# Optimization experiments

Hardware: AMD Instinct MI355X
Metric: run time of the kernel (lower is better)

The kernel has to match this reference:

```python
import jax, jax.numpy as jnp
import numpy as np

# --- config (matches init_kwargs) ---
NUM_EXPERTS = 8
TOP_K = 2
GROUP_DET = 1024
GROUP_CLS = 512
D_MODEL = 768
MLP_DIM = 3072


def setup_inputs() -> dict:
    key = jax.random.key(0)
    ks = jax.random.split(key, 8)
    scale = 0.02
    return {
        "x_det": jax.random.normal(ks[0], (16, 1024, D_MODEL), dtype=jnp.float32),
        "x_cls": jax.random.normal(ks[1], (16, 256, D_MODEL), dtype=jnp.float32),
        "w_router_det": jax.random.normal(ks[2], (D_MODEL, NUM_EXPERTS), dtype=jnp.float32) * scale,
        "w_router_cls": jax.random.normal(ks[3], (D_MODEL, NUM_EXPERTS), dtype=jnp.float32) * scale,
        "w1": jax.random.normal(ks[4], (NUM_EXPERTS, D_MODEL, MLP_DIM), dtype=jnp.float32) * scale,
        "b1": jnp.zeros((NUM_EXPERTS, MLP_DIM), dtype=jnp.float32),
        "w2": jax.random.normal(ks[5], (NUM_EXPERTS, MLP_DIM, D_MODEL), dtype=jnp.float32) * scale,
        "b2": jnp.zeros((NUM_EXPERTS, D_MODEL), dtype=jnp.float32),
    }


def _route(xg, w_router, top_k, num_experts, capacity):
    """Top-k per-item routing with expert capacity (vmoe-style einsum dispatcher).

    xg: [G, S, D] grouped tokens. Returns dispatch [G,S,E,C], combine [G,S,E,C].
    """
    G, S, _ = xg.shape
    gates = jax.nn.softmax(jnp.einsum("gsd,de->gse", xg, w_router))  # [G,S,E]
    gval, gidx = jax.lax.top_k(gates, top_k)  # [G,S,k]
    # k-major ordering: slot-0 choices of all tokens get capacity priority.
    mask = jax.nn.one_hot(gidx, num_experts, dtype=xg.dtype)  # [G,S,k,E]
    mask = mask.transpose(0, 2, 1, 3).reshape(G, top_k * S, num_experts)
    pos = jnp.cumsum(mask, axis=1) - 1.0  # position within expert buffer
    keep = mask * (pos < capacity)
    disp = keep[..., None] * jax.nn.one_hot(pos, capacity, dtype=xg.dtype)  # [G,kS,E,C]
    disp = disp.reshape(G, top_k, S, num_experts, capacity)
    combine = jnp.einsum("gksec,gks->gsec", disp, gval.transpose(0, 2, 1))
    dispatch = disp.sum(axis=1)  # [G,S,E,C] (one-hot: a token goes to each expert <=1 time)
    return dispatch, combine


def _expert_mlp(expert_in, w1, b1, w2, b2):
    # expert_in: [E, N, D] -> vmapped-expert MLP (grouped GEMM)
    h = jax.nn.gelu(jnp.einsum("end,edh->enh", expert_in, w1) + b1[:, None, :])
    return jnp.einsum("enh,ehd->end", h, w2) + b2[:, None, :]


def _moe(x, w_router, w1, b1, w2, b2, group_size):
    B, S, D = x.shape
    G = (B * S) // group_size
    capacity = (TOP_K * group_size) // NUM_EXPERTS
    xg = x.reshape(G, group_size, D)
    dispatch, combine = _route(xg, w_router, TOP_K, NUM_EXPERTS, capacity)
    expert_in = jnp.einsum("gsec,gsd->egcd", dispatch, xg)  # [E,G,C,D]
    E, _, C, _ = expert_in.shape
    y = _expert_mlp(expert_in.reshape(E, G * C, D), w1, b1, w2, b2).reshape(E, G, C, D)
    out = jnp.einsum("gsec,egcd->gsd", combine, y)
    return out.reshape(B, S, D)


def reference(x_det, x_cls, w_router_det, w_router_cls, w1, b1, w2, b2):
    out_det = _moe(x_det, w_router_det, w1, b1, w2, b2, GROUP_DET)
    out_cls = _moe(x_cls, w_router_cls, w1, b1, w2, b2, GROUP_CLS)
    # concatenate the two streams along the sequence axis for a single output
    return jnp.concatenate([out_det, out_cls], axis=1)
```

## Files before the change

### kernel.cpp

```cpp
#include <hip/hip_runtime.h>
#include <cstdint>
#include <cstddef>

#define NE 8
#define DMODEL 768
#define MLPDIM 3072
#define NDET 16384
#define NCLS 4096
#define NTOK 20480
#define ROWS_PER_E 5120
#define TOT_ROWS 40960

typedef float f32x4 __attribute__((ext_vector_type(4)));
typedef __bf16 bf16x8 __attribute__((ext_vector_type(8)));

__device__ __forceinline__ unsigned short f2bf(float f) {
    unsigned u = __float_as_uint(f);
    u += 0x7FFFu + ((u >> 16) & 1u);
    return (unsigned short)(u >> 16);
}
__device__ __forceinline__ float bf2f(unsigned v) {
    return __uint_as_float(v << 16);
}
__device__ __forceinline__ float gelu_f(float x) {
    float u = x * (0.7978845608028654f + 0.0356774081099f * x * x);
    return x * __frcp_rn(1.0f + __expf(-2.0f * u));
}

__device__ __forceinline__ void gload16(const void* g, void* l) {
    __builtin_amdgcn_global_load_lds(
        (const __attribute__((address_space(1))) unsigned int*)g,
        (__attribute__((address_space(3))) unsigned int*)l, 16, 0, 0);
}

__global__ void k_router(const float* __restrict__ xd, const float* __restrict__ xc,
                         const float* __restrict__ wrd, const float* __restrict__ wrc,
                         ushort* __restrict__ xbf,
                         int* __restrict__ e1, int* __restrict__ e2,
                         float* __restrict__ g1, float* __restrict__ g2) {
    int wave = threadIdx.x >> 6, lane = threadIdx.x & 63;
    int t = blockIdx.x * 4 + wave;
    if (t >= NTOK) return;
    const float* xrow;
    const float* w;
    if (t < NDET) { xrow = xd + (size_t)t * DMODEL; w = wrd; }
    else          { xrow = xc + (size_t)(t - NDET) * DMODEL; w = wrc; }
    ushort* xbrow = xbf + (size_t)t * DMODEL;
    float acc[8];
    #pragma unroll
    for (int e = 0; e < 8; e++) acc[e] = 0.0f;
    #pragma unroll
    for (int kk = 0; kk < DMODEL / 64; kk++) {
        int k = kk * 64 + lane;
        float xv = xrow[k];
        xbrow[k] = f2bf(xv);
        const float* wr = w + k * 8;
        #pragma unroll
        for (int e = 0; e < 8; e++) acc[e] += xv * wr[e];
    }
    #pragma unroll
    for (int e = 0; e < 8; e++) {
        #pragma unroll
        for (int off = 32; off > 0; off >>= 1) acc[e] += __shfl_xor(acc[e], off);
    }
    int i1 = 0; float v1 = acc[0];
    #pragma unroll
    for (int e = 1; e < 8; e++) if (acc[e] > v1) { v1 = acc[e]; i1 = e; }
    int i2 = -1; float v2 = -1e30f;
    #pragma unroll
    for (int e = 0; e < 8; e++) if (e != i1 && acc[e] > v2) { v2 = acc[e]; i2 = e; }
    float Z = 0.0f;
    #pragma unroll
    for (int e = 0; e < 8; e++) Z += __expf(acc[e] - v1);
    if (lane == 0) {
        e1[t] = i1; e2[t] = i2;
        g1[t] = 1.0f / Z;
        g2[t] = __expf(v2 - v1) / Z;
    }
}

__global__ void k_transpose_bf(const float* __restrict__ in, ushort* __restrict__ out,
                               int K, int N) {
    __shared__ float tile[32][33];
    int e = blockIdx.z;
    const float* A = in + (size_t)e * K * N;
    ushort* B = out + (size_t)e * N * K;
    int n0 = blockIdx.x * 32, k0 = blockIdx.y * 32;
    int tx = threadIdx.x, ty = threadIdx.y;
    float4 v = *(const float4*)(A + (size_t)(k0 + ty) * N + n0 + tx * 4);
    tile[ty][tx * 4 + 0] = v.x; tile[ty][tx * 4 + 1] = v.y;
    tile[ty][tx * 4 + 2] = v.z; tile[ty][tx * 4 + 3] = v.w;
    __syncthreads();
    ushort4 o;
    o.x = f2bf(tile[tx * 4 + 0][ty]);
    o.y = f2bf(tile[tx * 4 + 1][ty]);
    o.z = f2bf(tile[tx * 4 + 2][ty]);
    o.w = f2bf(tile[tx * 4 + 3][ty]);
    *(ushort4*)(B + (size_t)(n0 + ty) * K + k0 + tx * 4) = o;
}

__global__ void k_scan(const int* __restrict__ e1, const int* __restrict__ e2,
                       int* __restrict__ slot_map, int* __restrict__ r1, int* __restrict__ r2) {
    int g = blockIdx.x;
    int lane = threadIdx.x;
    int S, C, base;
    if (g < 16) { S = 1024; C = 256; base = g * 1024; }
    else        { S = 512;  C = 128; base = NDET + (g - 16) * 512; }
    int cnt[8];
    #pragma unroll
    for (int e = 0; e < 8; e++) cnt[e] = 0;
    unsigned long long lower = (lane == 0) ? 0ULL : ((~0ULL) >> (64 - lane));
    int nch = (2 * S) >> 6;
    for (int ch = 0; ch < nch; ch++) {
        int n = ch * 64 + lane;
        int k = (n >= S) ? 1 : 0;
        int s = n - k * S;
        int tok = base + s;
        int e = k ? e2[tok] : e1[tok];
        int pos = 0;
        #pragma unroll
        for (int ee = 0; ee < 8; ee++) {
            unsigned long long m = __ballot(e == ee);
            if (e == ee) pos = cnt[ee] + __popcll(m & lower);
            cnt[ee] += __popcll(m);
        }
        int r = -1;
        if (pos < C) {
            int local = (g < 16) ? (g * 256 + pos) : (4096 + (g - 16) * 128 + pos);
            r = e * ROWS_PER_E + local;
            slot_map[r] = tok;
        }
        if (k == 0) r1[tok] = r; else r2[tok] = r;
    }
}

template<int KTOT, int NTOT, int MODE, bool MFAST>
__global__ __launch_bounds__(256, 4) void k_gemm(
    const ushort* __restrict__ Asrc, const int* __restrict__ slot_map,
    const ushort* __restrict__ wtBase, const float* __restrict__ biasBase,
    ushort* __restrict__ Cdst, int eBase, int gm) {
    constexpr int KT = KTOT / 64;
    constexpr int NBN = NTOT / 128;
    __shared__ __align__(1024) ushort As[128 * 64];
    __shared__ __align__(1024) ushort Bs[128 * 64];

    const int q = gridDim.x >> 3;
    const int id2 = (blockIdx.x & 7) * q + (blockIdx.x >> 3);
    int mb, nb;
    if (MFAST) {
        int bpg = gm * NBN;
        int g = id2 / bpg, r = id2 - g * bpg;
        nb = r / gm;
        mb = g * gm + (r - nb * gm);
    } else {
        mb = id2 / NBN;
        nb = id2 - mb * NBN;
    }
    const int e = eBase + mb / (ROWS_PER_E / 128);
    const int m0 = mb * 128;
    const int rbase = eBase * ROWS_PER_E + m0;
    const int n0 = nb * 128;
    const ushort* Bt = wtBase + (size_t)e * KTOT * NTOT;
    const float* bias = biasBase + (size_t)e * NTOT;

    const int t = threadIdx.x, lane = t & 63, wave = t >> 6;
    const int g8 = lane >> 3;
    const int p8 = lane & 7;
    const int swz = ((p8 ^ g8) << 4);

    const char* aS[4];
    const char* bS[4];
    #pragma unroll
    for (int j = 0; j < 4; j++) {
        int r = wave * 32 + j * 8 + g8;
        size_t arow;
        if (MODE == 0) { int tk = slot_map[rbase + r]; arow = (size_t)(tk < 0 ? 0 : tk); }
        else           { arow = (size_t)(m0 + r); }
        aS[j] = (const char*)(Asrc + arow * KTOT) + swz;
        bS[j] = (const char*)(Bt + (size_t)(n0 + r) * KTOT) + swz;
    }

    auto ISSUE = [&](int kt) {
        size_t o = (size_t)kt * 128;
        #pragma unroll
        for (int j = 0; j < 4; j++) {
            gload16(aS[j] + o, As + (wave * 32 + j * 8) * 64);
            gload16(bS[j] + o, Bs + (wave * 32 + j * 8) * 64);
        }
    };

    const int wr = wave >> 1, wc = wave & 1;
    const int l15 = lane & 15, kq = lane >> 4, l7 = lane & 7;
    const int ch[2] = { ((kq) ^ l7) << 3, ((4 + kq) ^ l7) << 3 };

    f32x4 acc[4][4] = {};

    ISSUE(0);
    for (int ks = 0; ks < KT; ks++) {
        __syncthreads();
        bf16x8 af0[4], bf0[4];
        #pragma unroll
        for (int mi = 0; mi < 4; mi++)
            af0[mi] = *(const bf16x8*)(&As[(wr * 64 + mi * 16 + l15) * 64 + ch[0]]);
        #pragma unroll
        for (int nf = 0; nf < 4; nf++)
            bf0[nf] = *(const bf16x8*)(&Bs[(wc * 64 + nf * 16 + l15) * 64 + ch[0]]);
        __builtin_amdgcn_s_setprio(1);
        #pragma unroll
        for (int mi = 0; mi < 4; mi++) {
            #pragma unroll
            for (int nf = 0; nf < 4; nf++)
                acc[mi][nf] = __builtin_amdgcn_mfma_f32_16x16x32_bf16(
                    af0[mi], bf0[nf], acc[mi][nf], 0, 0, 0);
        }
        __builtin_amdgcn_s_setprio(0);
        bf16x8 af1[4], bf1[4];
        #pragma unroll
        for (int mi = 0; mi < 4; mi++)
            af1[mi] = *(const bf16x8*)(&As[(wr * 64 + mi * 16 + l15) * 64 + ch[1]]);
        #pragma unroll
        for (int nf = 0; nf < 4; nf++)
            bf1[nf] = *(const bf16x8*)(&Bs[(wc * 64 + nf * 16 + l15) * 64 + ch[1]]);
        __syncthreads();
        if (ks + 1 < KT) ISSUE(ks + 1);
        __builtin_amdgcn_s_setprio(1);
        #pragma unroll
        for (int mi = 0; mi < 4; mi++) {
            #pragma unroll
            for (int nf = 0; nf < 4; nf++)
                acc[mi][nf] = __builtin_amdgcn_mfma_f32_16x16x32_bf16(
                    af1[mi], bf1[nf], acc[mi][nf], 0, 0, 0);
        }
        __builtin_amdgcn_s_setprio(0);
    }

    const int ccolb = n0 + wc * 64 + l15;
    float bv[4];
    #pragma unroll
    for (int nf = 0; nf < 4; nf++) bv[nf] = bias[ccolb + nf * 16];

    const int rowb = (MODE == 0 ? m0 : rbase) + wr * 64 + (lane >> 4) * 4;
    #pragma unroll
    for (int mi = 0; mi < 4; mi++) {
        #pragma unroll
        for (int j = 0; j < 4; j++) {
            size_t roff = (size_t)(rowb + mi * 16 + j) * NTOT;
            #pragma unroll
            for (int nf = 0; nf < 4; nf++) {
                float v = acc[mi][nf][j] + bv[nf];
                if (MODE == 0) v = gelu_f(v);
                Cdst[roff + ccolb + nf * 16] = f2bf(v);
            }
        }
    }
}

__global__ void k_combine(const ushort* __restrict__ y,
                          const int* __restrict__ r1, const int* __restrict__ r2,
                          const float* __restrict__ g1, const float* __restrict__ g2,
                          float* __restrict__ out) {
    int t = blockIdx.x;
    int d = threadIdx.x;
    int a = r1[t], b = r2[t];
    float wa = g1[t], wb = g2[t];
    size_t opos;
    if (t < NDET) { int bb = t >> 10, s = t & 1023; opos = ((size_t)bb * 1280 + s) * 768; }
    else { int tt = t - NDET; int bb = tt >> 8, s = tt & 255; opos = ((size_t)bb * 1280 + 1024 + s) * 768; }
    int di = d * 4;
    float4 o = make_float4(0.f, 0.f, 0.f, 0.f);
    if (a >= 0) {
        uint2 v = *(const uint2*)(y + (size_t)a * 768 + di);
        o.x += wa * bf2f(v.x & 0xffffu); o.y += wa * bf2f(v.x >> 16);
        o.z += wa * bf2f(v.y & 0xffffu); o.w += wa * bf2f(v.y >> 16);
    }
    if (b >= 0) {
        uint2 v = *(const uint2*)(y + (size_t)b * 768 + di);
        o.x += wb * bf2f(v.x & 0xffffu); o.y += wb * bf2f(v.x >> 16);
        o.z += wb * bf2f(v.y & 0xffffu); o.w += wb * bf2f(v.y >> 16);
    }
    *(float4*)(out + opos + di) = o;
}

extern "C" void kernel_launch(void* const* d_in, const int* in_sizes, int n_in,
                              void* d_out, int out_size, void* d_ws, size_t ws_size,
                              hipStream_t stream) {
    const float* xd  = (const float*)d_in[0];
    const float* xc  = (const float*)d_in[1];
    const float* wrd = (const float*)d_in[2];
    const float* wrc = (const float*)d_in[3];
    const float* w1  = (const float*)d_in[4];
    const float* b1  = (const float*)d_in[5];
    const float* w2  = (const float*)d_in[6];
    const float* b2  = (const float*)d_in[7];
    float* out = (float*)d_out;

    size_t off = 0;
    char* base = (char*)d_ws;
    auto alloc = [&](size_t bytes) -> char* {
        char* r = base + off;
        off += (bytes + 255) & ~(size_t)255;
        return r;
    };
    ushort* xbf = (ushort*)alloc((size_t)NTOK * DMODEL * 2);
    ushort* w1t = (ushort*)alloc((size_t)NE * MLPDIM * DMODEL * 2);
    ushort* w2t = (ushort*)alloc((size_t)NE * DMODEL * MLPDIM * 2);
    ushort* y   = (ushort*)alloc((size_t)TOT_ROWS * DMODEL * 2);
    int*   slot_map = (int*)alloc((size_t)TOT_ROWS * 4);
    int*   e1 = (int*)alloc((size_t)NTOK * 4);
    int*   e2 = (int*)alloc((size_t)NTOK * 4);
    float* g1 = (float*)alloc((size_t)NTOK * 4);
    float* g2 = (float*)alloc((size_t)NTOK * 4);
    int*   r1 = (int*)alloc((size_t)NTOK * 4);
    int*   r2 = (int*)alloc((size_t)NTOK * 4);

    const size_t h_per_e = (size_t)ROWS_PER_E * MLPDIM * 2;
    int chunkE = 0;
    for (int c = NE; c >= 2; c >>= 1)
        if (off + c * h_per_e <= ws_size) { chunkE = c; break; }
    if (!chunkE) return;
    ushort* h = (ushort*)alloc((size_t)chunkE * h_per_e);

    hipMemsetAsync(slot_map, 0xFF, (size_t)TOT_ROWS * 4, stream);

    k_router<<<NTOK / 4, 256, 0, stream>>>(xd, xc, wrd, wrc, xbf, e1, e2, g1, g2);
    k_transpose_bf<<<dim3(MLPDIM / 32, DMODEL / 32, NE), dim3(8, 32), 0, stream>>>(w1, w1t, DMODEL, MLPDIM);
    k_transpose_bf<<<dim3(DMODEL / 32, MLPDIM / 32, NE), dim3(8, 32), 0, stream>>>(w2, w2t, MLPDIM, DMODEL);
    k_scan<<<24, 64, 0, stream>>>(e1, e2, slot_map, r1, r2);

    for (int e0 = 0; e0 < NE; e0 += chunkE) {
        int nmb = chunkE * (ROWS_PER_E / 128);
        int gm = (nmb % 20 == 0) ? 20 : 10;
        k_gemm<DMODEL, MLPDIM, 0, true><<<nmb * (MLPDIM / 128), 256, 0, stream>>>(
            xbf, slot_map, w1t, b1, h, e0, gm);
        k_gemm<MLPDIM, DMODEL, 1, false><<<nmb * (DMODEL / 128), 256, 0, stream>>>(
            h, slot_map, w2t, b2, y, e0, 0);
    }

    k_combine<<<NTOK, 192, 0, stream>>>(y, r1, r2, g1, g2, out);
}
```

Baseline: 569.2 us.

## Double-buffer LDS tiles with BK=32 to overlap global loads with MFMA

Replaces the single 64-deep K tile with two ping-pong 32-deep LDS buffers per operand, issuing the next stage's direct-to-LDS loads before computing on the current one. There is one barrier per K step instead of two, and the swizzle is adapted to the 32-wide rows. The goal is to hide global load latency behind MFMA work. The cost is twice as many loop iterations, a full vmcnt(0) wait each step, and a different LDS bank-conflict pattern. Total LDS usage stays the same.

```diff
diff --git a/kernel.cpp b/kernel.cpp
--- a/kernel.cpp
+++ b/kernel.cpp
@@ -139,10 +139,12 @@
     const ushort* __restrict__ Asrc, const int* __restrict__ slot_map,
     const ushort* __restrict__ wtBase, const float* __restrict__ biasBase,
     ushort* __restrict__ Cdst, int eBase, int gm) {
-    constexpr int KT = KTOT / 64;
+    constexpr int KT = KTOT / 32;
     constexpr int NBN = NTOT / 128;
-    __shared__ __align__(1024) ushort As[128 * 64];
-    __shared__ __align__(1024) ushort Bs[128 * 64];
+    __shared__ __align__(1024) ushort As0[128 * 32];
+    __shared__ __align__(1024) ushort As1[128 * 32];
+    __shared__ __align__(1024) ushort Bs0[128 * 32];
+    __shared__ __align__(1024) ushort Bs1[128 * 32];
 
     const int q = gridDim.x >> 3;
     const int id2 = (blockIdx.x & 7) * q + (blockIdx.x >> 3);
@@ -164,15 +166,15 @@
     const float* bias = biasBase + (size_t)e * NTOT;
 
     const int t = threadIdx.x, lane = t & 63, wave = t >> 6;
-    const int g8 = lane >> 3;
-    const int p8 = lane & 7;
-    const int swz = ((p8 ^ g8) << 4);
-
-    const char* aS[4];
-    const char* bS[4];
-    #pragma unroll
-    for (int j = 0; j < 4; j++) {
-        int r = wave * 32 + j * 8 + g8;
+    const int g16 = lane >> 2;
+    const int p4 = lane & 3;
+    const int swz = ((p4 ^ (g16 & 3)) << 4);
+
+    const char* aS[2];
+    const char* bS[2];
+    #pragma unroll
+    for (int j = 0; j < 2; j++) {
+        int r = wave * 32 + j * 16 + g16;
         size_t arow;
         if (MODE == 0) { int tk = slot_map[rbase + r]; arow = (size_t)(tk < 0 ? 0 : tk); }
         else           { arow = (size_t)(m0 + r); }
@@ -180,58 +182,53 @@
         bS[j] = (const char*)(Bt + (size_t)(n0 + r) * KTOT) + swz;
     }
 
-    auto ISSUE = [&](int kt) {
-        size_t o = (size_t)kt * 128;
-        #pragma unroll
-        for (int j = 0; j < 4; j++) {
-            gload16(aS[j] + o, As + (wave * 32 + j * 8) * 64);
-            gload16(bS[j] + o, Bs + (wave * 32 + j * 8) * 64);
+    auto STAGE = [&](int kt, ushort* WA, ushort* WB) {
+        size_t o = (size_t)kt * 64;
+        #pragma unroll
+        for (int j = 0; j < 2; j++) {
+            gload16(aS[j] + o, WA + (wave * 32 + j * 16) * 32);
+            gload16(bS[j] + o, WB + (wave * 32 + j * 16) * 32);
         }
     };
 
     const int wr = wave >> 1, wc = wave & 1;
-    const int l15 = lane & 15, kq = lane >> 4, l7 = lane & 7;
-    const int ch[2] = { ((kq) ^ l7) << 3, ((4 + kq) ^ l7) << 3 };
+    const int l15 = lane & 15, kq = lane >> 4;
+    const int ch = (kq ^ (l15 & 3)) << 3;
 
     f32x4 acc[4][4] = {};
 
-    ISSUE(0);
-    for (int ks = 0; ks < KT; ks++) {
-        __syncthreads();
-        bf16x8 af0[4], bf0[4];
+    auto BODY = [&](int kt, const ushort* RA, const ushort* RB, ushort* WA, ushort* WB) {
+        const bool last = (kt + 1 >= KT);
+        if (!last) STAGE(kt + 1, WA, WB);
+        bf16x8 af[4], bfr[4];
         #pragma unroll
         for (int mi = 0; mi < 4; mi++)
-            af0[mi] = *(const bf16x8*)(&As[(wr * 64 + mi * 16 + l15) * 64 + ch[0]]);
+            af[mi] = *(const bf16x8*)(&RA[(wr * 64 + mi * 16 + l15) * 32 + ch]);
         #pragma unroll
         for (int nf = 0; nf < 4; nf++)
-            bf0[nf] = *(const bf16x8*)(&Bs[(wc * 64 + nf * 16 + l15) * 64 + ch[0]]);
+            bfr[nf] = *(const bf16x8*)(&RB[(wc * 64 + nf * 16 + l15) * 32 + ch]);
         __builtin_amdgcn_s_setprio(1);
         #pragma unroll
         for (int mi = 0; mi < 4; mi++) {
             #pragma unroll
             for (int nf = 0; nf < 4; nf++)
                 acc[mi][nf] = __builtin_amdgcn_mfma_f32_16x16x32_bf16(
-                    af0[mi], bf0[nf], acc[mi][nf], 0, 0, 0);
+                    af[mi], bfr[nf], acc[mi][nf], 0, 0, 0);
         }
         __builtin_amdgcn_s_setprio(0);
-        bf16x8 af1[4], bf1[4];
-        #pragma unroll
-        for (int mi = 0; mi < 4; mi++)
-            af1[mi] = *(const bf16x8*)(&As[(wr * 64 + mi * 16 + l15) * 64 + ch[1]]);
-        #pragma unroll
-        for (int nf = 0; nf < 4; nf++)
-            bf1[nf] = *(const bf16x8*)(&Bs[(wc * 64 + nf * 16 + l15) * 64 + ch[1]]);
-        __syncthreads();
-        if (ks + 1 < KT) ISSUE(ks + 1);
-        __builtin_amdgcn_s_setprio(1);
-        #pragma unroll
-        for (int mi = 0; mi < 4; mi++) {
-            #pragma unroll
-            for (int nf = 0; nf < 4; nf++)
-                acc[mi][nf] = __builtin_amdgcn_mfma_f32_16x16x32_bf16(
-                    af1[mi], bf1[nf], acc[mi][nf], 0, 0, 0);
-        }
-        __builtin_amdgcn_s_setprio(0);
+        if (!last) {
+            asm volatile("s_waitcnt vmcnt(0)" ::: "memory");
+            __builtin_amdgcn_s_barrier();
+        }
+    };
+
+    STAGE(0, As0, Bs0);
+    asm volatile("s_waitcnt vmcnt(0)" ::: "memory");
+    __builtin_amdgcn_s_barrier();
+
+    for (int kt = 0; kt < KT; kt += 2) {
+        BODY(kt,     As0, Bs0, As1, Bs1);
+        BODY(kt + 1, As1, Bs1, As0, Bs0);
     }
 
     const int ccolb = n0 + wc * 64 + l15;
```

Result: slower. 639.8 us (+12.4%).
